# Optimization experiments

Hardware: AMD Instinct MI355X
Metric: run time of the kernel (lower is better)

Reference implementation:

```python
import jax, jax.numpy as jnp
import numpy as np

WINDOW = 11
C1 = 0.01 ** 2
C2 = 0.03 ** 2
PAD = WINDOW // 2


def _box_filter(img, kernel):
    # img: [B,1,H,W], kernel: [1,1,w,w]; SAME padding (odd window)
    return jax.lax.conv_general_dilated(
        img, kernel,
        window_strides=(1, 1),
        padding=[(PAD, PAD), (PAD, PAD)],
        dimension_numbers=('NCHW', 'OIHW', 'NCHW'))


def setup_inputs() -> dict:
    key = jax.random.key(0)
    kx, ky = jax.random.split(key)
    B, C, H, W = 64, 1, 512, 512
    x = jax.random.uniform(kx, (B, C, H, W), dtype=jnp.float32)
    y = jax.random.uniform(ky, (B, C, H, W), dtype=jnp.float32)
    kernel = jnp.ones((1, 1, WINDOW, WINDOW), dtype=jnp.float32) / (WINDOW ** 2)
    return {"x": x, "y": y, "kernel": kernel}


def reference(x, y, kernel):
    mu_x = _box_filter(x, kernel)
    mu_y = _box_filter(y, kernel)
    mu_x2 = mu_x * mu_x
    mu_y2 = mu_y * mu_y
    mu_xy = mu_x * mu_y
    sigma_x2 = _box_filter(x * x, kernel) - mu_x2
    sigma_y2 = _box_filter(y * y, kernel) - mu_y2
    sigma_xy = _box_filter(x * y, kernel) - mu_xy
    ssim_map = ((2.0 * mu_xy + C1) * (2.0 * sigma_xy + C2)) / (
        (mu_x2 + mu_y2 + C1) * (sigma_x2 + sigma_y2 + C2))
    return 1.0 - jnp.mean(ssim_map)
```

## Files before the change

### kernel.cpp

```cpp
#include <hip/hip_runtime.h>
#include <stdint.h>


#define IMG_H 512
#define IMG_W 512
#define N_IMG 64
#define BAND  64
#define NBANDG 8
#define NBLOCKS (N_IMG * NBANDG)
#define NSLOT 19
#define NSTEP 22

#define SLOT_BYTES 4096
#define Y0_OFF 2048

#define C1S2 1.4641f
#define C2S2 13.1769f

typedef __attribute__((address_space(3))) uint32_t lds_u32_t;
typedef const __attribute__((address_space(1))) uint32_t glb_u32_t;

__device__ __forceinline__ void dma16(void* lds, const void* g) {
    __builtin_amdgcn_global_load_lds((glb_u32_t*)g, (lds_u32_t*)lds, 16, 0, 0);
}

__device__ __forceinline__ float dpp_shr1(float v) {
    return __int_as_float(__builtin_amdgcn_update_dpp(
        0, __float_as_int(v), 0x138, 0xF, 0xF, true));
}
__device__ __forceinline__ float dpp_shl1(float v) {
    return __int_as_float(__builtin_amdgcn_update_dpp(
        0, __float_as_int(v), 0x130, 0xF, 0xF, true));
}

__device__ __forceinline__ int wrapS(int s) { return s >= NSLOT ? s - NSLOT : s; }

__global__ __launch_bounds__(192) void ssim_fused(const float* __restrict__ x,
                                                  const float* __restrict__ y,
                                                  float* __restrict__ part)
{
    __shared__ __align__(16) char ring[NSLOT][SLOT_BYTES];

    const int tx = threadIdx.x & 63;
    const int wv = threadIdx.x >> 6;

    const int wid = (blockIdx.x & 7) * (NBLOCKS / 8) + (blockIdx.x >> 3);
    const int img = wid >> 3;
    const int bg  = wid & (NBANDG - 1);
    const int r0  = bg * BAND;
    const int q0  = r0 + wv;

    const float* __restrict__ xi = x + (size_t)img * (IMG_H * IMG_W);
    const float* __restrict__ yi = y + (size_t)img * (IMG_H * IMG_W);

    auto dma_row = [&](int slot, int ri) {
        int rc = ri < 0 ? 0 : (ri > IMG_H - 1 ? IMG_H - 1 : ri);
        char* s = &ring[slot][0];
        const char* xg = (const char*)(xi + (size_t)rc * IMG_W) + tx * 16;
        const char* yg = (const char*)(yi + (size_t)rc * IMG_W) + tx * 16;
        dma16(s,          xg);
        dma16(s + 1024,   xg + 1024);
        dma16(s + Y0_OFF, yg);
        dma16(s + Y0_OFF + 1024, yg + 1024);
    };

    float Vx[8], Vy[8], Vss[8], Vxy[8];
#pragma unroll
    for (int j = 0; j < 8; ++j) { Vx[j] = 0.f; Vy[j] = 0.f; Vss[j] = 0.f; Vxy[j] = 0.f; }

    auto accum_add = [&](const char* s) {
        const float4* xr = (const float4*)(s + (size_t)tx * 32);
        const float4* yr = (const float4*)(s + Y0_OFF + (size_t)tx * 32);
        float4 x0 = xr[0], x1 = xr[1];
        float4 y0 = yr[0], y1 = yr[1];
        float xs[8] = {x0.x, x0.y, x0.z, x0.w, x1.x, x1.y, x1.z, x1.w};
        float ys[8] = {y0.x, y0.y, y0.z, y0.w, y1.x, y1.y, y1.z, y1.w};
#pragma unroll
        for (int j = 0; j < 8; ++j) {
            Vx[j] += xs[j];
            Vy[j] += ys[j];
            Vss[j] = fmaf(xs[j], xs[j], Vss[j]);
            Vss[j] = fmaf(ys[j], ys[j], Vss[j]);
            Vxy[j] = fmaf(xs[j], ys[j], Vxy[j]);
        }
    };

    auto accum_sub = [&](const char* s) {
        const float4* xr = (const float4*)(s + (size_t)tx * 32);
        const float4* yr = (const float4*)(s + Y0_OFF + (size_t)tx * 32);
        float4 x0 = xr[0], x1 = xr[1];
        float4 y0 = yr[0], y1 = yr[1];
        float xs[8] = {x0.x, x0.y, x0.z, x0.w, x1.x, x1.y, x1.z, x1.w};
        float ys[8] = {y0.x, y0.y, y0.z, y0.w, y1.x, y1.y, y1.z, y1.w};
#pragma unroll
        for (int j = 0; j < 8; ++j) {
            Vx[j]  -= xs[j];
            Vy[j]  -= ys[j];
            Vss[j] = fmaf(-xs[j], xs[j], Vss[j]);
            Vss[j] = fmaf(-ys[j], ys[j], Vss[j]);
            Vxy[j] = fmaf(-xs[j], ys[j], Vxy[j]);
        }
    };

    auto hsum = [&](const float (&V)[8], float (&S)[8]) {
        float w[18];
#pragma unroll
        for (int k = 0; k < 5; ++k) w[k] = dpp_shr1(V[3 + k]);
#pragma unroll
        for (int j = 0; j < 8; ++j) w[5 + j] = V[j];
#pragma unroll
        for (int k = 0; k < 5; ++k) w[13 + k] = dpp_shl1(V[k]);
        float s0 = (w[0] + w[1]) + (w[2] + w[3]);
        float s1 = (w[4] + w[5]) + (w[6] + w[7]);
        float s2 = (w[8] + w[9]) + w[10];
        float s  = (s0 + s1) + s2;
        S[0] = s;
#pragma unroll
        for (int j = 1; j < 8; ++j) { s += w[j + 10] - w[j - 1]; S[j] = s; }
    };

    auto ssim8 = [&](const float (&Sx)[8], const float (&Sy)[8],
                     const float (&Sss)[8], const float (&Sxy)[8],
                     float& loss) {
#pragma unroll
        for (int j = 0; j < 8; ++j) {
            float A  = Sx[j] * Sy[j];
            float B  = fmaf(Sx[j], Sx[j], Sy[j] * Sy[j]);
            float n1 = fmaf(A, 2.0f, C1S2);
            float n2 = fmaf(Sxy[j], 242.0f, fmaf(A, -2.0f, C2S2));
            float d1 = B + C1S2;
            float d2 = fmaf(Sss[j], 121.0f, C2S2 - B);
            loss += __fdividef(n1 * n2, d1 * d2);
        }
    };

#pragma unroll 1
    for (int k = wv; k < 16; k += 3) dma_row(k + 1, r0 - 8 + k);
    __syncthreads();
#pragma unroll 1
    for (int t = 0; t < 11; ++t) {
        int row = q0 - 8 + t;
        if (row >= 0) accum_add(&ring[wv + 1 + t][0]);
    }

    float loss = 0.0f;
    int c = 0;

#pragma unroll 1
    for (int i = 0; i < NSTEP; ++i) {
        const int base = r0 + 3 * i;
        const int q = base + wv;
        const bool act = (3 * i + wv) < BAND;

        if (act) {
            if (q - 8 >= 0) accum_sub(&ring[wrapS(c + 1 + wv)][0]);
            if (q - 7 >= 0) accum_sub(&ring[wrapS(c + 2 + wv)][0]);
            if (q - 6 >= 0) accum_sub(&ring[wrapS(c + 3 + wv)][0]);
            if (q + 3 < IMG_H) accum_add(&ring[wrapS(c + 12 + wv)][0]);
            if (q + 4 < IMG_H) accum_add(&ring[wrapS(c + 13 + wv)][0]);
            if (q + 5 < IMG_H) accum_add(&ring[wrapS(c + 14 + wv)][0]);
        }

        if (i < NSTEP - 1) dma_row(wrapS(c + 17 + wv), base + 8 + wv);

        if (act) {
            float Sx[8], Sy[8], Sss[8], Sxy[8];
            hsum(Vx, Sx); hsum(Vy, Sy); hsum(Vss, Sss); hsum(Vxy, Sxy);
            ssim8(Sx, Sy, Sss, Sxy, loss);
        }

        c = wrapS(c + 3);
        __syncthreads();
    }

#pragma unroll
    for (int off = 32; off > 0; off >>= 1)
        loss += __shfl_down(loss, off, 64);

    float* pr = reinterpret_cast<float*>(&ring[0][0]);
    if (tx == 0) pr[wv] = loss;
    __syncthreads();
    if (threadIdx.x == 0)
        part[blockIdx.x] = (pr[0] + pr[1]) + pr[2];
}

__global__ __launch_bounds__(256) void ssim_reduce(const float* __restrict__ part,
                                                   float* __restrict__ out)
{
    const int t  = threadIdx.x;
    const int tx = t & 63;
    float s = part[t] + part[t + 256];
#pragma unroll
    for (int off = 32; off > 0; off >>= 1)
        s += __shfl_down(s, off, 64);
    __shared__ float ws[4];
    if (tx == 0) ws[t >> 6] = s;
    __syncthreads();
    if (t == 0) {
        float total = (ws[0] + ws[1]) + (ws[2] + ws[3]);
        out[0] = 1.0f - total * (1.0f / ((float)N_IMG * IMG_H * IMG_W));
    }
}

extern "C" void kernel_launch(void* const* d_in, const int* in_sizes, int n_in,
                              void* d_out, int out_size, void* d_ws, size_t ws_size,
                              hipStream_t stream) {
    const float* x = (const float*)d_in[0];
    const float* y = (const float*)d_in[1];
    float* part = (float*)d_ws;

    ssim_fused<<<NBLOCKS, 192, 0, stream>>>(x, y, part);
    ssim_reduce<<<1, 256, 0, stream>>>(part, (float*)d_out);
}
```

Measured before the change: 166.9 us.

## Replace LDS DMA ring with per-wave register ring of rows

Drops the shared-memory ring buffer, the global-to-LDS DMA loads and the per-step block barriers. Each single-wave block now keeps a 12-row register window of x and y, loading rows directly from global memory into registers while sliding a vertical box sum over a 32-row band. Band size halves and the block count doubles, and partial sums are accumulated with atomics into a zeroed buffer. The register arrays raise VGPR pressure and latency hiding now depends on occupancy instead of explicit prefetch, while the vertical halo reload overhead rises with the shorter bands.

```diff
diff --git a/kernel.cpp b/kernel.cpp
--- a/kernel.cpp
+++ b/kernel.cpp
@@ -5,24 +5,12 @@
 #define IMG_H 512
 #define IMG_W 512
 #define N_IMG 64
-#define BAND  64
-#define NBANDG 8
+#define BAND  32
+#define NBANDG 16
 #define NBLOCKS (N_IMG * NBANDG)
-#define NSLOT 19
-#define NSTEP 22
-
-#define SLOT_BYTES 4096
-#define Y0_OFF 2048
 
 #define C1S2 1.4641f
 #define C2S2 13.1769f
-
-typedef __attribute__((address_space(3))) uint32_t lds_u32_t;
-typedef const __attribute__((address_space(1))) uint32_t glb_u32_t;
-
-__device__ __forceinline__ void dma16(void* lds, const void* g) {
-    __builtin_amdgcn_global_load_lds((glb_u32_t*)g, (lds_u32_t*)lds, 16, 0, 0);
-}
 
 __device__ __forceinline__ float dpp_shr1(float v) {
     return __int_as_float(__builtin_amdgcn_update_dpp(
@@ -33,74 +21,55 @@
         0, __float_as_int(v), 0x130, 0xF, 0xF, true));
 }
 
-__device__ __forceinline__ int wrapS(int s) { return s >= NSLOT ? s - NSLOT : s; }
-
-__global__ __launch_bounds__(192) void ssim_fused(const float* __restrict__ x,
-                                                  const float* __restrict__ y,
-                                                  float* __restrict__ part)
+__global__ __launch_bounds__(64) void ssim_fused(const float* __restrict__ x,
+                                                 const float* __restrict__ y,
+                                                 float* __restrict__ part)
 {
-    __shared__ __align__(16) char ring[NSLOT][SLOT_BYTES];
-
-    const int tx = threadIdx.x & 63;
-    const int wv = threadIdx.x >> 6;
-
+    const int tx = threadIdx.x;
     const int wid = (blockIdx.x & 7) * (NBLOCKS / 8) + (blockIdx.x >> 3);
-    const int img = wid >> 3;
+    const int img = wid >> 4;
     const int bg  = wid & (NBANDG - 1);
     const int r0  = bg * BAND;
-    const int q0  = r0 + wv;
+    const int c0  = tx * 8;
 
-    const float* __restrict__ xi = x + (size_t)img * (IMG_H * IMG_W);
-    const float* __restrict__ yi = y + (size_t)img * (IMG_H * IMG_W);
+    const float* __restrict__ xi = x + (size_t)img * (IMG_H * IMG_W) + c0;
+    const float* __restrict__ yi = y + (size_t)img * (IMG_H * IMG_W) + c0;
 
-    auto dma_row = [&](int slot, int ri) {
-        int rc = ri < 0 ? 0 : (ri > IMG_H - 1 ? IMG_H - 1 : ri);
-        char* s = &ring[slot][0];
-        const char* xg = (const char*)(xi + (size_t)rc * IMG_W) + tx * 16;
-        const char* yg = (const char*)(yi + (size_t)rc * IMG_W) + tx * 16;
-        dma16(s,          xg);
-        dma16(s + 1024,   xg + 1024);
-        dma16(s + Y0_OFF, yg);
-        dma16(s + Y0_OFF + 1024, yg + 1024);
-    };
-
+    float X[12][8], Y[12][8];
     float Vx[8], Vy[8], Vss[8], Vxy[8];
 #pragma unroll
     for (int j = 0; j < 8; ++j) { Vx[j] = 0.f; Vy[j] = 0.f; Vss[j] = 0.f; Vxy[j] = 0.f; }
 
-    auto accum_add = [&](const char* s) {
-        const float4* xr = (const float4*)(s + (size_t)tx * 32);
-        const float4* yr = (const float4*)(s + Y0_OFF + (size_t)tx * 32);
-        float4 x0 = xr[0], x1 = xr[1];
-        float4 y0 = yr[0], y1 = yr[1];
-        float xs[8] = {x0.x, x0.y, x0.z, x0.w, x1.x, x1.y, x1.z, x1.w};
-        float ys[8] = {y0.x, y0.y, y0.z, y0.w, y1.x, y1.y, y1.z, y1.w};
-#pragma unroll
-        for (int j = 0; j < 8; ++j) {
-            Vx[j] += xs[j];
-            Vy[j] += ys[j];
-            Vss[j] = fmaf(xs[j], xs[j], Vss[j]);
-            Vss[j] = fmaf(ys[j], ys[j], Vss[j]);
-            Vxy[j] = fmaf(xs[j], ys[j], Vxy[j]);
-        }
-    };
+#define LOADROW(u, rowv) do {                                             \
+        int rc_ = (rowv);                                                 \
+        rc_ = rc_ < 0 ? 0 : (rc_ > IMG_H - 1 ? IMG_H - 1 : rc_);          \
+        const float4* px_ = (const float4*)(xi + (size_t)rc_ * IMG_W);    \
+        const float4* py_ = (const float4*)(yi + (size_t)rc_ * IMG_W);    \
+        float4 a_ = px_[0], b_ = px_[1];                                  \
+        float4 c_ = py_[0], d_ = py_[1];                                  \
+        X[u][0] = a_.x; X[u][1] = a_.y; X[u][2] = a_.z; X[u][3] = a_.w;   \
+        X[u][4] = b_.x; X[u][5] = b_.y; X[u][6] = b_.z; X[u][7] = b_.w;   \
+        Y[u][0] = c_.x; Y[u][1] = c_.y; Y[u][2] = c_.z; Y[u][3] = c_.w;   \
+        Y[u][4] = d_.x; Y[u][5] = d_.y; Y[u][6] = d_.z; Y[u][7] = d_.w;   \
+    } while (0)
 
-    auto accum_sub = [&](const char* s) {
-        const float4* xr = (const float4*)(s + (size_t)tx * 32);
-        const float4* yr = (const float4*)(s + Y0_OFF + (size_t)tx * 32);
-        float4 x0 = xr[0], x1 = xr[1];
-        float4 y0 = yr[0], y1 = yr[1];
-        float xs[8] = {x0.x, x0.y, x0.z, x0.w, x1.x, x1.y, x1.z, x1.w};
-        float ys[8] = {y0.x, y0.y, y0.z, y0.w, y1.x, y1.y, y1.z, y1.w};
-#pragma unroll
-        for (int j = 0; j < 8; ++j) {
-            Vx[j]  -= xs[j];
-            Vy[j]  -= ys[j];
-            Vss[j] = fmaf(-xs[j], xs[j], Vss[j]);
-            Vss[j] = fmaf(-ys[j], ys[j], Vss[j]);
-            Vxy[j] = fmaf(-xs[j], ys[j], Vxy[j]);
-        }
-    };
+#define ADDS(s) do { _Pragma("unroll")                                    \
+        for (int j = 0; j < 8; ++j) {                                     \
+            Vx[j] += X[s][j];                                             \
+            Vy[j] += Y[s][j];                                             \
+            Vss[j] = fmaf(X[s][j], X[s][j], Vss[j]);                      \
+            Vss[j] = fmaf(Y[s][j], Y[s][j], Vss[j]);                      \
+            Vxy[j] = fmaf(X[s][j], Y[s][j], Vxy[j]);                      \
+        } } while (0)
+
+#define SUBS(s) do { _Pragma("unroll")                                    \
+        for (int j = 0; j < 8; ++j) {                                     \
+            Vx[j] -= X[s][j];                                             \
+            Vy[j] -= Y[s][j];                                             \
+            Vss[j] = fmaf(-X[s][j], X[s][j], Vss[j]);                     \
+            Vss[j] = fmaf(-Y[s][j], Y[s][j], Vss[j]);                     \
+            Vxy[j] = fmaf(-X[s][j], Y[s][j], Vxy[j]);                     \
+        } } while (0)
 
     auto hsum = [&](const float (&V)[8], float (&S)[8]) {
         float w[18];
@@ -119,69 +88,54 @@
         for (int j = 1; j < 8; ++j) { s += w[j + 10] - w[j - 1]; S[j] = s; }
     };
 
-    auto ssim8 = [&](const float (&Sx)[8], const float (&Sy)[8],
-                     const float (&Sss)[8], const float (&Sxy)[8],
-                     float& loss) {
+    float loss = 0.0f;
+
+#define SSIM8() do { _Pragma("unroll")                                    \
+        for (int j = 0; j < 8; ++j) {                                     \
+            float A  = Sx[j] * Sy[j];                                     \
+            float B  = fmaf(Sx[j], Sx[j], Sy[j] * Sy[j]);                 \
+            float n1 = fmaf(A, 2.0f, C1S2);                               \
+            float n2 = fmaf(Sxy[j], 242.0f, fmaf(A, -2.0f, C2S2));        \
+            float d1 = B + C1S2;                                          \
+            float d2 = fmaf(Sss[j], 121.0f, C2S2 - B);                    \
+            loss += __fdividef(n1 * n2, d1 * d2);                         \
+        } } while (0)
+
+#define STEP(u) do {                                                      \
+        const int r_ = rb + (u);                                          \
+        if (r_ - 6 >= 0) SUBS(u);                                         \
+        LOADROW(u, r_ + 6);                                               \
+        if (r_ + 5 < IMG_H) ADDS(((u) + 11) % 12);                        \
+        float Sx[8], Sy[8], Sss[8], Sxy[8];                               \
+        hsum(Vx, Sx); hsum(Vy, Sy); hsum(Vss, Sss); hsum(Vxy, Sxy);       \
+        SSIM8();                                                          \
+    } while (0)
+
 #pragma unroll
-        for (int j = 0; j < 8; ++j) {
-            float A  = Sx[j] * Sy[j];
-            float B  = fmaf(Sx[j], Sx[j], Sy[j] * Sy[j]);
-            float n1 = fmaf(A, 2.0f, C1S2);
-            float n2 = fmaf(Sxy[j], 242.0f, fmaf(A, -2.0f, C2S2));
-            float d1 = B + C1S2;
-            float d2 = fmaf(Sss[j], 121.0f, C2S2 - B);
-            loss += __fdividef(n1 * n2, d1 * d2);
-        }
-    };
+    for (int k = 0; k < 12; ++k) LOADROW(k, r0 - 6 + k);
+#pragma unroll
+    for (int k = 0; k < 11; ++k) {
+        if (r0 - 6 + k >= 0) ADDS(k);
+    }
 
 #pragma unroll 1
-    for (int k = wv; k < 16; k += 3) dma_row(k + 1, r0 - 8 + k);
-    __syncthreads();
-#pragma unroll 1
-    for (int t = 0; t < 11; ++t) {
-        int row = q0 - 8 + t;
-        if (row >= 0) accum_add(&ring[wv + 1 + t][0]);
+    for (int g = 0; g < 2; ++g) {
+        const int rb = r0 + 12 * g;
+        STEP(0);  STEP(1);  STEP(2);  STEP(3);
+        STEP(4);  STEP(5);  STEP(6);  STEP(7);
+        STEP(8);  STEP(9);  STEP(10); STEP(11);
     }
-
-    float loss = 0.0f;
-    int c = 0;
-
-#pragma unroll 1
-    for (int i = 0; i < NSTEP; ++i) {
-        const int base = r0 + 3 * i;
-        const int q = base + wv;
-        const bool act = (3 * i + wv) < BAND;
-
-        if (act) {
-            if (q - 8 >= 0) accum_sub(&ring[wrapS(c + 1 + wv)][0]);
-            if (q - 7 >= 0) accum_sub(&ring[wrapS(c + 2 + wv)][0]);
-            if (q - 6 >= 0) accum_sub(&ring[wrapS(c + 3 + wv)][0]);
-            if (q + 3 < IMG_H) accum_add(&ring[wrapS(c + 12 + wv)][0]);
-            if (q + 4 < IMG_H) accum_add(&ring[wrapS(c + 13 + wv)][0]);
-            if (q + 5 < IMG_H) accum_add(&ring[wrapS(c + 14 + wv)][0]);
-        }
-
-        if (i < NSTEP - 1) dma_row(wrapS(c + 17 + wv), base + 8 + wv);
-
-        if (act) {
-            float Sx[8], Sy[8], Sss[8], Sxy[8];
-            hsum(Vx, Sx); hsum(Vy, Sy); hsum(Vss, Sss); hsum(Vxy, Sxy);
-            ssim8(Sx, Sy, Sss, Sxy, loss);
-        }
-
-        c = wrapS(c + 3);
-        __syncthreads();
+    {
+        const int rb = r0 + 24;
+        STEP(0); STEP(1); STEP(2); STEP(3);
+        STEP(4); STEP(5); STEP(6); STEP(7);
     }
 
 #pragma unroll
     for (int off = 32; off > 0; off >>= 1)
         loss += __shfl_down(loss, off, 64);
-
-    float* pr = reinterpret_cast<float*>(&ring[0][0]);
-    if (tx == 0) pr[wv] = loss;
-    __syncthreads();
-    if (threadIdx.x == 0)
-        part[blockIdx.x] = (pr[0] + pr[1]) + pr[2];
+    if (tx == 0)
+        atomicAdd(&part[blockIdx.x & 511], loss);
 }
 
 __global__ __launch_bounds__(256) void ssim_reduce(const float* __restrict__ part,
@@ -209,6 +163,7 @@
     const float* y = (const float*)d_in[1];
     float* part = (float*)d_ws;
 
-    ssim_fused<<<NBLOCKS, 192, 0, stream>>>(x, y, part);
+    hipMemsetAsync(part, 0, 512 * sizeof(float), stream);
+    ssim_fused<<<NBLOCKS, 64, 0, stream>>>(x, y, part);
     ssim_reduce<<<1, 256, 0, stream>>>(part, (float*)d_out);
 }
```

Measured after the change: 191.5 us. 14.7% more time.
